# Kernel optimization log

Hardware: AMD Instinct MI355X
Metric: run time of the kernel (lower is better)

The kernel has to match this reference:

```python
import jax, jax.numpy as jnp
import numpy as np

H = 512
V = 8000

def _attn(hidden, enc, W, b, v):
    # hidden: [1,B,H], enc: [T,B,H] -> context [1,B,H]
    encB = jnp.transpose(enc, (1, 0, 2))                      # [B,T,H]
    Hrep = jnp.broadcast_to(jnp.transpose(hidden, (1, 0, 2)), encB.shape)
    energy = jnp.tanh(jnp.concatenate([Hrep, encB], axis=-1) @ W.T + b)  # [B,T,H]
    scores = jnp.einsum('bth,h->bt', energy, v)               # [B,T]
    a = jax.nn.softmax(scores, axis=1)
    ctx = jnp.einsum('bt,bth->bh', a, encB)                   # [B,H]
    return ctx[None]

def _gru_step(x, h, W_ih, W_hh, b_ih, b_hh):
    # x: [B,in], h: [B,H]; PyTorch gate order r,z,n
    gi = x @ W_ih.T + b_ih
    gh = h @ W_hh.T + b_hh
    i_r, i_z, i_n = jnp.split(gi, 3, axis=1)
    h_r, h_z, h_n = jnp.split(gh, 3, axis=1)
    r = jax.nn.sigmoid(i_r + h_r)
    z = jax.nn.sigmoid(i_z + h_z)
    n = jnp.tanh(i_n + r * h_n)
    return (1.0 - z) * n + z * h

def setup_inputs() -> dict:
    key = jax.random.key(0)
    ks = jax.random.split(key, 20)
    B, Tz, Tu, E, D = 128, 64, 128, 512, 5
    gin = E + 2 * H + D  # 1541
    s = 0.02  # small init scale to keep tanh/sigmoid unsaturated
    return {
        'z_enc_out': jax.random.normal(ks[0], (Tz, B, H), jnp.float32),
        'u_enc_out': jax.random.normal(ks[1], (Tu, B, H), jnp.float32),
        'm_t_input': jax.random.randint(ks[2], (1, B), 0, V),
        'degree_input': jax.random.uniform(ks[3], (B, D), jnp.float32),
        'last_hidden': jax.random.normal(ks[4], (1, B, H), jnp.float32),
        'sparse_response': jax.random.uniform(ks[5], (B, Tz, V + Tz), jnp.float32, 1e-3, 1.0),
        'emb_table': jax.random.normal(ks[6], (V, E), jnp.float32) * s,
        'attn_z_W': jax.random.normal(ks[7], (H, 2 * H), jnp.float32) * s,
        'attn_z_b': jnp.zeros((H,), jnp.float32),
        'attn_z_v': jax.random.normal(ks[8], (H,), jnp.float32) * s,
        'attn_u_W': jax.random.normal(ks[9], (H, 2 * H), jnp.float32) * s,
        'attn_u_b': jnp.zeros((H,), jnp.float32),
        'attn_u_v': jax.random.normal(ks[10], (H,), jnp.float32) * s,
        'gru_W_ih': jax.random.normal(ks[11], (3 * H, gin), jnp.float32) * s,
        'gru_W_hh': jax.random.normal(ks[12], (3 * H, H), jnp.float32) * s,
        'gru_b_ih': jnp.zeros((3 * H,), jnp.float32),
        'gru_b_hh': jnp.zeros((3 * H,), jnp.float32),
        'proj_W': jax.random.normal(ks[13], (V, 3 * H), jnp.float32) * s,
        'proj_b': jnp.zeros((V,), jnp.float32),
        'copy2_W': jax.random.normal(ks[14], (H, H), jnp.float32) * s,
        'copy2_b': jnp.zeros((H,), jnp.float32),
    }

def reference(z_enc_out, u_enc_out, m_t_input, degree_input, last_hidden,
              sparse_response, emb_table, attn_z_W, attn_z_b, attn_z_v,
              attn_u_W, attn_u_b, attn_u_v, gru_W_ih, gru_W_hh, gru_b_ih,
              gru_b_hh, proj_W, proj_b, copy2_W, copy2_b):
    m_embed = emb_table[m_t_input]                                 # [1,B,E]
    z_ctx = _attn(last_hidden, z_enc_out, attn_z_W, attn_z_b, attn_z_v)  # [1,B,H]
    u_ctx = _attn(last_hidden, u_enc_out, attn_u_W, attn_u_b, attn_u_v)  # [1,B,H]
    gru_in = jnp.concatenate([m_embed, u_ctx, z_ctx, degree_input[None]], axis=2)
    h_new = _gru_step(gru_in[0], last_hidden[0], gru_W_ih, gru_W_hh, gru_b_ih, gru_b_hh)  # [B,H]
    gru_out = h_new[None]                                          # [1,B,H]
    gen_score = (jnp.concatenate([z_ctx, u_ctx, gru_out], axis=2)[0] @ proj_W.T + proj_b)  # [B,V]
    # copy scores over z encoder positions
    zT = jnp.transpose(z_enc_out, (1, 0, 2))                       # [B,Tz,H]
    cs = jnp.tanh(zT @ copy2_W.T + copy2_b)                        # [B,Tz,H]
    z_score = jnp.einsum('bth,bh->bt', cs, h_new)                  # [B,Tz]
    m = jnp.max(z_score, axis=1, keepdims=True)
    e = jnp.exp(z_score - m)
    z_copy = jnp.log(jnp.einsum('bt,btv->bv', e, sparse_response)) + m  # [B,V+Tz]
    scores = jax.nn.softmax(jnp.concatenate([gen_score, z_copy], axis=1), axis=1)
    gen, cp = scores[:, :V], scores[:, V:]
    proba = jnp.concatenate([gen + cp[:, :V], cp[:, V:]], axis=1)  # [B,V+Tz]
    return proba, gru_out, gru_out
```

## Files before the change

kernel.cpp:

```cpp
#include <hip/hip_runtime.h>
#include <hip/hip_bf16.h>
#include <math.h>

#define B_   128
#define H_   512
#define TZ   64
#define TU   128
#define V_   8000
#define VC   8064
#define GIN  1541
#define GINP 1568
#define G3   1536
#define NB   8

typedef float f32x4 __attribute__((ext_vector_type(4)));
typedef __bf16 bf16x8 __attribute__((ext_vector_type(8)));

__device__ __forceinline__ float sigmoidf_(float x){ return 1.f/(1.f+__expf(-x)); }

__device__ __forceinline__ void cvt8(const float* __restrict__ s, __bf16* __restrict__ d){
  float4 x = *(const float4*)s;
  float4 y = *(const float4*)(s+4);
  bf16x8 r;
  r[0]=(__bf16)x.x; r[1]=(__bf16)x.y; r[2]=(__bf16)x.z; r[3]=(__bf16)x.w;
  r[4]=(__bf16)y.x; r[5]=(__bf16)y.y; r[6]=(__bf16)y.z; r[7]=(__bf16)y.w;
  *(bf16x8*)d = r;
}

#define U_Z   524288u
#define U_U   1048576u
#define U_H   8192u
#define U_ZW  65536u
#define U_UW  65536u
#define U_CW  32768u
#define U_WHH 98304u
#define U_PW  1536000u
#define U_WIH 301056u
#define CVT_UNITS (U_Z+U_U+U_H+U_ZW+U_UW+U_CW+U_WHH+U_PW+U_WIH)

__global__ __launch_bounds__(256) void cvt_all(
    const float* __restrict__ z, const float* __restrict__ u, const float* __restrict__ hid,
    const float* __restrict__ zW, const float* __restrict__ uW, const float* __restrict__ cW,
    const float* __restrict__ whh, const float* __restrict__ pW, const float* __restrict__ wih,
    __bf16* __restrict__ zb, __bf16* __restrict__ ub, __bf16* __restrict__ hb,
    __bf16* __restrict__ zWb, __bf16* __restrict__ uWb, __bf16* __restrict__ cWb,
    __bf16* __restrict__ whhb, __bf16* __restrict__ pWb, __bf16* __restrict__ Wp)
{
  unsigned t = blockIdx.x*256u + threadIdx.x;
  if (t >= CVT_UNITS) return;
  unsigned o = t;
  if (o >= CVT_UNITS - U_WIH) {
    o -= (CVT_UNITS - U_WIH);
    unsigned r = o / (GINP/8), cu = o % (GINP/8);
    int c0 = cu*8;
    const float* src = wih + (size_t)r*GIN;
    bf16x8 v;
#pragma unroll
    for (int e = 0; e < 8; ++e) {
      int c = c0 + e;
      v[e] = (__bf16)((c < GIN) ? src[c] : 0.f);
    }
    *(bf16x8*)(Wp + (size_t)r*GINP + c0) = v;
    return;
  }
  const float* s; __bf16* d;
  if      (o < U_Z)                   { s=z;   d=zb;   }
  else if ((o-=U_Z)   < U_U)          { s=u;   d=ub;   }
  else if ((o-=U_U)   < U_H)          { s=hid; d=hb;   }
  else if ((o-=U_H)   < U_ZW)         { s=zW;  d=zWb;  }
  else if ((o-=U_ZW)  < U_UW)         { s=uW;  d=uWb;  }
  else if ((o-=U_UW)  < U_CW)         { s=cW;  d=cWb;  }
  else if ((o-=U_CW)  < U_WHH)        { s=whh; d=whhb; }
  else     { o-=U_WHH;                  s=pW;  d=pWb;  }
  cvt8(s + (size_t)o*8, d + (size_t)o*8);
}

__global__ __launch_bounds__(256) void hidden3(
    const __bf16* __restrict__ hb,
    const __bf16* __restrict__ zWb, const float* __restrict__ zbias, float* __restrict__ hWz,
    const __bf16* __restrict__ uWb, const float* __restrict__ ubias, float* __restrict__ hWu,
    const __bf16* __restrict__ whhb, const float* __restrict__ hbias, float* __restrict__ gh)
{
  const int wv = threadIdx.x >> 6, lane = threadIdx.x & 63;
  const int tile = blockIdx.x*4 + wv;
  if (tile >= 80) return;
  const __bf16* W; const float* bias; float* C; int ldw, ldc, nbn, lt;
  if (tile < 16)      { W=zWb;  bias=zbias; C=hWz; ldw=2*H_; ldc=H_; nbn=8;  lt=tile; }
  else if (tile < 32) { W=uWb;  bias=ubias; C=hWu; ldw=2*H_; ldc=H_; nbn=8;  lt=tile-16; }
  else                { W=whhb; bias=hbias; C=gh;  ldw=H_;   ldc=G3; nbn=24; lt=tile-32; }
  const int bn = (lt % nbn) * 64, bm = (lt / nbn) * 64;
  const int col = lane & 15, g = lane >> 4;
  f32x4 acc[4][4] = {};
  for (int k0 = 0; k0 < 512; k0 += 32) {
    const int k = k0 + g*8;
    bf16x8 af[4], bw[4];
#pragma unroll
    for (int i = 0; i < 4; ++i) {
      af[i] = *(const bf16x8*)(hb + (size_t)(bm + i*16 + col)*H_ + k);
      bw[i] = *(const bf16x8*)(W  + (size_t)(bn + i*16 + col)*ldw + k);
    }
#pragma unroll
    for (int i = 0; i < 4; ++i)
#pragma unroll
      for (int j = 0; j < 4; ++j)
        acc[i][j] = __builtin_amdgcn_mfma_f32_16x16x32_bf16(af[i], bw[j], acc[i][j], 0, 0, 0);
  }
#pragma unroll
  for (int mi = 0; mi < 4; ++mi)
#pragma unroll
    for (int r = 0; r < 4; ++r) {
      int m = bm + mi*16 + g*4 + r;
#pragma unroll
      for (int ni = 0; ni < 4; ++ni) {
        int n = bn + ni*16 + col;
        C[(size_t)m*ldc + n] = acc[mi][ni][r] + bias[n];
      }
    }
}

__global__ __launch_bounds__(256) void mfma_energy2(
    const __bf16* __restrict__ Az, const __bf16* __restrict__ Wz, int ldwz,
    const float* __restrict__ addz, int asz, const float* __restrict__ mulz, int msz,
    float* __restrict__ outz, int Tz,
    const __bf16* __restrict__ Au, const __bf16* __restrict__ Wu, int ldwu,
    const float* __restrict__ addu, int asu, const float* __restrict__ mulu, int msu,
    float* __restrict__ outu, int Tu,
    int ztiles, int ntiles)
{
  const int wv = threadIdx.x >> 6, lane = threadIdx.x & 63;
  const int tile = blockIdx.x*4 + wv;
  if (tile >= ntiles) return;
  const __bf16 *A, *W; const float *add, *mul; float* outp;
  int ldw, as, ms, T, lt;
  if (tile < ztiles) { A=Az; W=Wz; ldw=ldwz; add=addz; as=asz; mul=mulz; ms=msz; outp=outz; T=Tz; lt=tile; }
  else               { A=Au; W=Wu; ldw=ldwu; add=addu; as=asu; mul=mulu; ms=msu; outp=outu; T=Tu; lt=tile-ztiles; }
  const int nb = lt & 7;
  const int bn = nb * 64, bm = (lt >> 3) * 64;
  const int col = lane & 15, g = lane >> 4;
  f32x4 acc[4][4] = {};
  for (int k0 = 0; k0 < 512; k0 += 32) {
    const int k = k0 + g*8;
    bf16x8 af[4], bw[4];
#pragma unroll
    for (int i = 0; i < 4; ++i) {
      af[i] = *(const bf16x8*)(A + (size_t)(bm + i*16 + col)*512 + k);
      bw[i] = *(const bf16x8*)(W + (size_t)(bn + i*16 + col)*ldw + k);
    }
#pragma unroll
    for (int i = 0; i < 4; ++i)
#pragma unroll
      for (int j = 0; j < 4; ++j)
        acc[i][j] = __builtin_amdgcn_mfma_f32_16x16x32_bf16(af[i], bw[j], acc[i][j], 0, 0, 0);
  }
#pragma unroll
  for (int mi = 0; mi < 4; ++mi)
#pragma unroll
    for (int r = 0; r < 4; ++r) {
      int m = bm + mi*16 + g*4 + r;
      int b = m & (B_-1), t = m >> 7;
      float p = 0.f;
#pragma unroll
      for (int ni = 0; ni < 4; ++ni) {
        int n = bn + ni*16 + col;
        float v = tanhf(acc[mi][ni][r] + add[(size_t)b*as + n]);
        p += v * mul[(size_t)b*ms + n];
      }
      p += __shfl_xor(p, 1); p += __shfl_xor(p, 2);
      p += __shfl_xor(p, 4); p += __shfl_xor(p, 8);
      if (col == 0) outp[(size_t)nb*(B_*T) + b*T + t] = p;
    }
}

__global__ __launch_bounds__(256) void attn_ctx_concat(
    const float* __restrict__ partZ, const float* __restrict__ partU,
    const __bf16* __restrict__ zb, const __bf16* __restrict__ ub,
    const int* __restrict__ m_t, const float* __restrict__ emb,
    const float* __restrict__ degree,
    __bf16* __restrict__ gin, __bf16* __restrict__ cat3b)
{
  const int b = blockIdx.x, tid = threadIdx.x;
  __shared__ float sa[256];
  __shared__ float awz[TZ];
  __shared__ float awu[TU];
  {
    float s = -INFINITY;
    if (tid < TZ) {
      s = 0.f;
#pragma unroll
      for (int nb = 0; nb < NB; ++nb) s += partZ[(size_t)nb*(B_*TZ) + b*TZ + tid];
    }
    sa[tid] = s; __syncthreads();
    for (int o = 128; o > 0; o >>= 1) { if (tid < o) sa[tid] = fmaxf(sa[tid], sa[tid+o]); __syncthreads(); }
    float mx = sa[0]; __syncthreads();
    float e = (tid < TZ) ? __expf(s - mx) : 0.f;
    sa[tid] = e; __syncthreads();
    for (int o = 128; o > 0; o >>= 1) { if (tid < o) sa[tid] += sa[tid+o]; __syncthreads(); }
    float inv = 1.f / sa[0];
    if (tid < TZ) awz[tid] = e * inv;
    __syncthreads();
  }
  {
    float s = -INFINITY;
    if (tid < TU) {
      s = 0.f;
#pragma unroll
      for (int nb = 0; nb < NB; ++nb) s += partU[(size_t)nb*(B_*TU) + b*TU + tid];
    }
    sa[tid] = s; __syncthreads();
    for (int o = 128; o > 0; o >>= 1) { if (tid < o) sa[tid] = fmaxf(sa[tid], sa[tid+o]); __syncthreads(); }
    float mx = sa[0]; __syncthreads();
    float e = (tid < TU) ? __expf(s - mx) : 0.f;
    sa[tid] = e; __syncthreads();
    for (int o = 128; o > 0; o >>= 1) { if (tid < o) sa[tid] += sa[tid+o]; __syncthreads(); }
    float inv = 1.f / sa[0];
    if (tid < TU) awu[tid] = e * inv;
    __syncthreads();
  }
  const float* e = emb + (size_t)m_t[b] * H_;
  for (int h = tid; h < H_; h += 256) {
    float accz = 0.f, accu = 0.f;
    for (int t = 0; t < TZ; ++t) accz += awz[t] * (float)zb[((size_t)t*B_ + b)*H_ + h];
    for (int t = 0; t < TU; ++t) accu += awu[t] * (float)ub[((size_t)t*B_ + b)*H_ + h];
    gin[(size_t)b*GINP + h]          = (__bf16)e[h];
    gin[(size_t)b*GINP + H_ + h]     = (__bf16)accu;
    gin[(size_t)b*GINP + 2*H_ + h]   = (__bf16)accz;
    cat3b[(size_t)b*G3 + h]          = (__bf16)accz;
    cat3b[(size_t)b*G3 + H_ + h]     = (__bf16)accu;
  }
  if (tid < 5) gin[(size_t)b*GINP + 3*H_ + tid] = (__bf16)degree[b*5 + tid];
  if (tid >= 5 && tid < 32) gin[(size_t)b*GINP + GIN + (tid-5)] = (__bf16)0.f;
}

__global__ __launch_bounds__(256) void mfma_gru(
    const __bf16* __restrict__ A, const __bf16* __restrict__ W,
    float* __restrict__ giA, float* __restrict__ giB)
{
  const int wv = threadIdx.x >> 6, lane = threadIdx.x & 63;
  const int tile = blockIdx.x*4 + wv;
  if (tile >= 96) return;
  const int half = tile / 48, lt = tile % 48;
  const int bn = (lt % 24) * 64, bm = (lt / 24) * 64;
  const int col = lane & 15, g = lane >> 4;
  const int kbeg = half ? 800 : 0, kend_ = half ? GINP : 800;
  float* C = half ? giB : giA;
  f32x4 acc[4][4] = {};
  for (int k0 = kbeg; k0 < kend_; k0 += 32) {
    const int k = k0 + g*8;
    bf16x8 af[4], bw[4];
#pragma unroll
    for (int i = 0; i < 4; ++i) {
      af[i] = *(const bf16x8*)(A + (size_t)(bm + i*16 + col)*GINP + k);
      bw[i] = *(const bf16x8*)(W + (size_t)(bn + i*16 + col)*GINP + k);
    }
#pragma unroll
    for (int i = 0; i < 4; ++i)
#pragma unroll
      for (int j = 0; j < 4; ++j)
        acc[i][j] = __builtin_amdgcn_mfma_f32_16x16x32_bf16(af[i], bw[j], acc[i][j], 0, 0, 0);
  }
#pragma unroll
  for (int mi = 0; mi < 4; ++mi)
#pragma unroll
    for (int r = 0; r < 4; ++r) {
      int m = bm + mi*16 + g*4 + r;
#pragma unroll
      for (int ni = 0; ni < 4; ++ni)
        C[(size_t)m*G3 + bn + ni*16 + col] = acc[mi][ni][r];
    }
}

__global__ __launch_bounds__(256) void gru_kernel(
    const float* __restrict__ giA, const float* __restrict__ giB,
    const float* __restrict__ gh, const float* __restrict__ bih,
    const float* __restrict__ hprev,
    float* __restrict__ hnew, __bf16* __restrict__ cat3b,
    float* __restrict__ out1, float* __restrict__ out2)
{
  int idx = blockIdx.x*256 + threadIdx.x;
  int b = idx >> 9, h = idx & (H_-1);
  size_t base = (size_t)b*G3;
  float ir = giA[base + h]        + giB[base + h]        + bih[h]        + gh[base + h];
  float iz = giA[base + H_ + h]   + giB[base + H_ + h]   + bih[H_ + h]   + gh[base + H_ + h];
  float in_= giA[base + 2*H_ + h] + giB[base + 2*H_ + h] + bih[2*H_ + h];
  float hn = gh[base + 2*H_ + h];
  float r = sigmoidf_(ir);
  float z = sigmoidf_(iz);
  float n = tanhf(in_ + r*hn);
  float hv = (1.f - z)*n + z*hprev[idx];
  hnew[idx] = hv;
  cat3b[base + 2*H_ + h] = (__bf16)hv;
  out1[idx] = hv;
  out2[idx] = hv;
}

__global__ __launch_bounds__(256) void proj_copy(
    const __bf16* __restrict__ cat3b, const __bf16* __restrict__ pWb, float* __restrict__ P,
    const __bf16* __restrict__ zb, const __bf16* __restrict__ cWb,
    const float* __restrict__ c2b, const float* __restrict__ hnew,
    float* __restrict__ partC)
{
  const int wv = threadIdx.x >> 6, lane = threadIdx.x & 63;
  const int tile = blockIdx.x*4 + wv;
  const int col = lane & 15, g = lane >> 4;
  if (tile < 750) {
    const int s = tile / 250, t2 = tile % 250;
    const int bn = (t2 % 125) * 64, bm = (t2 / 125) * 64;
    const __bf16* As = cat3b + s*512;
    const __bf16* Ws = pWb + s*512;
    float* C = P + (size_t)s*B_*V_;
    f32x4 acc[4][4] = {};
    for (int k0 = 0; k0 < 512; k0 += 32) {
      const int k = k0 + g*8;
      bf16x8 af[4], bw[4];
#pragma unroll
      for (int i = 0; i < 4; ++i) {
        af[i] = *(const bf16x8*)(As + (size_t)(bm + i*16 + col)*G3 + k);
        bw[i] = *(const bf16x8*)(Ws + (size_t)(bn + i*16 + col)*G3 + k);
      }
#pragma unroll
      for (int i = 0; i < 4; ++i)
#pragma unroll
        for (int j = 0; j < 4; ++j)
          acc[i][j] = __builtin_amdgcn_mfma_f32_16x16x32_bf16(af[i], bw[j], acc[i][j], 0, 0, 0);
    }
#pragma unroll
    for (int mi = 0; mi < 4; ++mi)
#pragma unroll
      for (int r = 0; r < 4; ++r) {
        int m = bm + mi*16 + g*4 + r;
#pragma unroll
        for (int ni = 0; ni < 4; ++ni)
          C[(size_t)m*V_ + bn + ni*16 + col] = acc[mi][ni][r];
      }
  } else if (tile < 750 + 1024) {
    const int lt = tile - 750;
    const int nb = lt & 7;
    const int bn = nb * 64, bm = (lt >> 3) * 64;
    f32x4 acc[4][4] = {};
    for (int k0 = 0; k0 < 512; k0 += 32) {
      const int k = k0 + g*8;
      bf16x8 af[4], bw[4];
#pragma unroll
      for (int i = 0; i < 4; ++i) {
        af[i] = *(const bf16x8*)(zb + (size_t)(bm + i*16 + col)*512 + k);
        bw[i] = *(const bf16x8*)(cWb + (size_t)(bn + i*16 + col)*H_ + k);
      }
#pragma unroll
      for (int i = 0; i < 4; ++i)
#pragma unroll
        for (int j = 0; j < 4; ++j)
          acc[i][j] = __builtin_amdgcn_mfma_f32_16x16x32_bf16(af[i], bw[j], acc[i][j], 0, 0, 0);
    }
#pragma unroll
    for (int mi = 0; mi < 4; ++mi)
#pragma unroll
      for (int r = 0; r < 4; ++r) {
        int m = bm + mi*16 + g*4 + r;
        int b = m & (B_-1), t = m >> 7;
        float p = 0.f;
#pragma unroll
        for (int ni = 0; ni < 4; ++ni) {
          int n = bn + ni*16 + col;
          float v = tanhf(acc[mi][ni][r] + c2b[n]);
          p += v * hnew[(size_t)b*H_ + n];
        }
        p += __shfl_xor(p, 1); p += __shfl_xor(p, 2);
        p += __shfl_xor(p, 4); p += __shfl_xor(p, 8);
        if (col == 0) partC[(size_t)nb*(B_*TZ) + b*TZ + t] = p;
      }
  }
}

__global__ __launch_bounds__(256) void zcopy_kernel(
    const float* __restrict__ partC, const float* __restrict__ sr,
    float* __restrict__ zbuf)
{
  const int b = blockIdx.y, tid = threadIdx.x;
  __shared__ float se[TZ];
  __shared__ float smx;
  if (tid < TZ) {
    float s = 0.f;
#pragma unroll
    for (int nb = 0; nb < NB; ++nb) s += partC[(size_t)nb*(B_*TZ) + b*TZ + tid];
    float mx = s;
    mx = fmaxf(mx, __shfl_xor(mx, 1));  mx = fmaxf(mx, __shfl_xor(mx, 2));
    mx = fmaxf(mx, __shfl_xor(mx, 4));  mx = fmaxf(mx, __shfl_xor(mx, 8));
    mx = fmaxf(mx, __shfl_xor(mx, 16)); mx = fmaxf(mx, __shfl_xor(mx, 32));
    se[tid] = __expf(s - mx);
    if (tid == 0) smx = mx;
  }
  __syncthreads();
  const int v0 = blockIdx.x*1024 + tid*4;
  if (v0 >= VC) return;
  float4 acc = {0.f, 0.f, 0.f, 0.f};
  const float* base = sr + (size_t)b*TZ*VC;
#pragma unroll 4
  for (int t = 0; t < TZ; ++t) {
    float et = se[t];
    float4 x = *(const float4*)(base + (size_t)t*VC + v0);
    acc.x += et*x.x; acc.y += et*x.y; acc.z += et*x.z; acc.w += et*x.w;
  }
  float m = smx;
  float* out = zbuf + (size_t)b*VC + v0;
  out[0] = __logf(acc.x) + m;
  out[1] = __logf(acc.y) + m;
  out[2] = __logf(acc.z) + m;
  out[3] = __logf(acc.w) + m;
}

__global__ __launch_bounds__(256) void final_softmax2(
    const float* __restrict__ p0, const float* __restrict__ p1, const float* __restrict__ p2,
    const float* __restrict__ bias, const float* __restrict__ zbuf, float* __restrict__ out0)
{
  const int b = blockIdx.x, tid = threadIdx.x;
  const float* q0 = p0 + (size_t)b*V_;
  const float* q1 = p1 + (size_t)b*V_;
  const float* q2 = p2 + (size_t)b*V_;
  const float* zr = zbuf + (size_t)b*VC;
  __shared__ float sa[256];
  float mx = -INFINITY;
  for (int i = tid; i < V_; i += 256) mx = fmaxf(mx, q0[i]+q1[i]+q2[i]+bias[i]);
  for (int i = tid; i < VC; i += 256) mx = fmaxf(mx, zr[i]);
  sa[tid] = mx; __syncthreads();
  for (int o = 128; o > 0; o >>= 1) { if (tid < o) sa[tid] = fmaxf(sa[tid], sa[tid+o]); __syncthreads(); }
  mx = sa[0]; __syncthreads();
  float sum = 0.f;
  for (int i = tid; i < V_; i += 256) sum += __expf(q0[i]+q1[i]+q2[i]+bias[i] - mx);
  for (int i = tid; i < VC; i += 256) sum += __expf(zr[i] - mx);
  sa[tid] = sum; __syncthreads();
  for (int o = 128; o > 0; o >>= 1) { if (tid < o) sa[tid] += sa[tid+o]; __syncthreads(); }
  float inv = 1.f / sa[0];
  float* o0 = out0 + (size_t)b*VC;
  for (int j = tid; j < V_; j += 256)
    o0[j] = (__expf(q0[j]+q1[j]+q2[j]+bias[j]-mx) + __expf(zr[j]-mx)) * inv;
  for (int j = tid; j < TZ; j += 256)
    o0[V_ + j] = __expf(zr[V_ + j] - mx) * inv;
}

extern "C" void kernel_launch(void* const* d_in, const int* in_sizes, int n_in,
                              void* d_out, int out_size, void* d_ws, size_t ws_size,
                              hipStream_t stream)
{
  const float* z_enc   = (const float*)d_in[0];
  const float* u_enc   = (const float*)d_in[1];
  const int*   m_t     = (const int*)  d_in[2];
  const float* degree  = (const float*)d_in[3];
  const float* hidden  = (const float*)d_in[4];
  const float* sr      = (const float*)d_in[5];
  const float* emb     = (const float*)d_in[6];
  const float* attn_z_W= (const float*)d_in[7];
  const float* attn_z_b= (const float*)d_in[8];
  const float* attn_z_v= (const float*)d_in[9];
  const float* attn_u_W= (const float*)d_in[10];
  const float* attn_u_b= (const float*)d_in[11];
  const float* attn_u_v= (const float*)d_in[12];
  const float* gru_W_ih= (const float*)d_in[13];
  const float* gru_W_hh= (const float*)d_in[14];
  const float* gru_b_ih= (const float*)d_in[15];
  const float* gru_b_hh= (const float*)d_in[16];
  const float* proj_W  = (const float*)d_in[17];
  const float* proj_b  = (const float*)d_in[18];
  const float* copy2_W = (const float*)d_in[19];
  const float* copy2_b = (const float*)d_in[20];

  float* out0 = (float*)d_out;
  float* out1 = out0 + (size_t)B_*VC;
  float* out2 = out1 + (size_t)B_*H_;

  float* ws    = (float*)d_ws;
  float* hWz   = ws;
  float* hWu   = hWz   + B_*H_;
  float* gh    = hWu   + B_*H_;
  float* partZ = gh    + B_*G3;
  float* partU = partZ + NB*B_*TZ;
  float* partC = partU + NB*B_*TU;
  float* giA   = partC + NB*B_*TZ;
  float* giB   = giA   + B_*G3;
  float* hnew  = giB   + B_*G3;
  float* p0    = hnew  + B_*H_;
  float* p1    = p0    + (size_t)B_*V_;
  float* p2    = p1    + (size_t)B_*V_;
  float* zbuf  = p2    + (size_t)B_*V_;
  __bf16* gin   = (__bf16*)(zbuf + (size_t)B_*VC);
  __bf16* Wp    = gin   + (size_t)B_*GINP;
  __bf16* zb    = Wp    + (size_t)G3*GINP;
  __bf16* ub    = zb    + (size_t)TZ*B_*H_;
  __bf16* hb    = ub    + (size_t)TU*B_*H_;
  __bf16* zWb   = hb    + (size_t)B_*H_;
  __bf16* uWb   = zWb   + (size_t)H_*2*H_;
  __bf16* cWb   = uWb   + (size_t)H_*2*H_;
  __bf16* whhb  = cWb   + (size_t)H_*H_;
  __bf16* pWb   = whhb  + (size_t)G3*H_;
  __bf16* cat3b = pWb   + (size_t)V_*G3;

  cvt_all<<<(CVT_UNITS + 255)/256, 256, 0, stream>>>(
      z_enc, u_enc, hidden, attn_z_W, attn_u_W, copy2_W, gru_W_hh, proj_W, gru_W_ih,
      zb, ub, hb, zWb, uWb, cWb, whhb, pWb, Wp);

  hidden3<<<20, 256, 0, stream>>>(hb, zWb, attn_z_b, hWz, uWb, attn_u_b, hWu, whhb, gru_b_hh, gh);

  mfma_energy2<<<768, 256, 0, stream>>>(
      zb, zWb + H_, 2*H_, hWz, H_, attn_z_v, 0, partZ, TZ,
      ub, uWb + H_, 2*H_, hWu, H_, attn_u_v, 0, partU, TU,
      1024, 3072);

  attn_ctx_concat<<<B_, 256, 0, stream>>>(partZ, partU, zb, ub, m_t, emb, degree, gin, cat3b);

  mfma_gru<<<24, 256, 0, stream>>>(gin, Wp, giA, giB);
  gru_kernel<<<(B_*H_)/256, 256, 0, stream>>>(giA, giB, gh, gru_b_ih, hidden, hnew, cat3b, out1, out2);

  proj_copy<<<444, 256, 0, stream>>>(cat3b, pWb, p0, zb, cWb, copy2_b, hnew, partC);

  zcopy_kernel<<<dim3((VC + 1023)/1024, B_), 256, 0, stream>>>(partC, sr, zbuf);

  final_softmax2<<<B_, 256, 0, stream>>>(p0, p1, p2, proj_b, zbuf, out0);
}
```

Before: 295.2 us.

## Convert projection weights to bf16 inside proj GEMM and cover full batch per tile

Stops pre-converting the large proj_W matrix to bf16 in cvt_all. The projection GEMM now reads fp32 weights directly and converts them in registers. Each wave now covers all 128 batch rows (8x4 MFMA tiles), so every weight tile is loaded once rather than twice. This removes a separate write and re-read of about 24 MB of bf16 weights, at the cost of doubled accumulator registers per wave, fewer tiles and blocks, and fp32 weight loads that are twice as wide.

```diff
diff --git a/kernel.cpp b/kernel.cpp
--- a/kernel.cpp
+++ b/kernel.cpp
@@ -18,13 +18,16 @@
 
 __device__ __forceinline__ float sigmoidf_(float x){ return 1.f/(1.f+__expf(-x)); }
 
-__device__ __forceinline__ void cvt8(const float* __restrict__ s, __bf16* __restrict__ d){
-  float4 x = *(const float4*)s;
-  float4 y = *(const float4*)(s+4);
+__device__ __forceinline__ bf16x8 load8_bf16(const float* __restrict__ p){
+  float4 x = *(const float4*)p;
+  float4 y = *(const float4*)(p+4);
   bf16x8 r;
   r[0]=(__bf16)x.x; r[1]=(__bf16)x.y; r[2]=(__bf16)x.z; r[3]=(__bf16)x.w;
   r[4]=(__bf16)y.x; r[5]=(__bf16)y.y; r[6]=(__bf16)y.z; r[7]=(__bf16)y.w;
-  *(bf16x8*)d = r;
+  return r;
+}
+__device__ __forceinline__ void cvt8(const float* __restrict__ s, __bf16* __restrict__ d){
+  *(bf16x8*)d = load8_bf16(s);
 }
 
 #define U_Z   524288u
@@ -34,17 +37,16 @@
 #define U_UW  65536u
 #define U_CW  32768u
 #define U_WHH 98304u
-#define U_PW  1536000u
 #define U_WIH 301056u
-#define CVT_UNITS (U_Z+U_U+U_H+U_ZW+U_UW+U_CW+U_WHH+U_PW+U_WIH)
+#define CVT_UNITS (U_Z+U_U+U_H+U_ZW+U_UW+U_CW+U_WHH+U_WIH)
 
 __global__ __launch_bounds__(256) void cvt_all(
     const float* __restrict__ z, const float* __restrict__ u, const float* __restrict__ hid,
     const float* __restrict__ zW, const float* __restrict__ uW, const float* __restrict__ cW,
-    const float* __restrict__ whh, const float* __restrict__ pW, const float* __restrict__ wih,
+    const float* __restrict__ whh, const float* __restrict__ wih,
     __bf16* __restrict__ zb, __bf16* __restrict__ ub, __bf16* __restrict__ hb,
     __bf16* __restrict__ zWb, __bf16* __restrict__ uWb, __bf16* __restrict__ cWb,
-    __bf16* __restrict__ whhb, __bf16* __restrict__ pWb, __bf16* __restrict__ Wp)
+    __bf16* __restrict__ whhb, __bf16* __restrict__ Wp)
 {
   unsigned t = blockIdx.x*256u + threadIdx.x;
   if (t >= CVT_UNITS) return;
@@ -70,8 +72,7 @@
   else if ((o-=U_H)   < U_ZW)         { s=zW;  d=zWb;  }
   else if ((o-=U_ZW)  < U_UW)         { s=uW;  d=uWb;  }
   else if ((o-=U_UW)  < U_CW)         { s=cW;  d=cWb;  }
-  else if ((o-=U_CW)  < U_WHH)        { s=whh; d=whhb; }
-  else     { o-=U_WHH;                  s=pW;  d=pWb;  }
+  else     { o-=U_CW;                   s=whh; d=whhb; }
   cvt8(s + (size_t)o*8, d + (size_t)o*8);
 }
 
@@ -294,7 +295,7 @@
 }
 
 __global__ __launch_bounds__(256) void proj_copy(
-    const __bf16* __restrict__ cat3b, const __bf16* __restrict__ pWb, float* __restrict__ P,
+    const __bf16* __restrict__ cat3b, const float* __restrict__ pW, float* __restrict__ P,
     const __bf16* __restrict__ zb, const __bf16* __restrict__ cWb,
     const float* __restrict__ c2b, const float* __restrict__ hnew,
     float* __restrict__ partC)
@@ -302,38 +303,39 @@
   const int wv = threadIdx.x >> 6, lane = threadIdx.x & 63;
   const int tile = blockIdx.x*4 + wv;
   const int col = lane & 15, g = lane >> 4;
-  if (tile < 750) {
-    const int s = tile / 250, t2 = tile % 250;
-    const int bn = (t2 % 125) * 64, bm = (t2 / 125) * 64;
+  if (tile < 375) {
+    const int s = tile / 125;
+    const int bn = (tile % 125) * 64;
     const __bf16* As = cat3b + s*512;
-    const __bf16* Ws = pWb + s*512;
+    const float*  Ws = pW + s*512;
     float* C = P + (size_t)s*B_*V_;
-    f32x4 acc[4][4] = {};
+    f32x4 acc[8][4] = {};
     for (int k0 = 0; k0 < 512; k0 += 32) {
       const int k = k0 + g*8;
-      bf16x8 af[4], bw[4];
-#pragma unroll
-      for (int i = 0; i < 4; ++i) {
-        af[i] = *(const bf16x8*)(As + (size_t)(bm + i*16 + col)*G3 + k);
-        bw[i] = *(const bf16x8*)(Ws + (size_t)(bn + i*16 + col)*G3 + k);
-      }
+      bf16x8 af[8], bw[4];
+#pragma unroll
+      for (int i = 0; i < 8; ++i)
+        af[i] = *(const bf16x8*)(As + (size_t)(i*16 + col)*G3 + k);
 #pragma unroll
       for (int i = 0; i < 4; ++i)
-#pragma unroll
-        for (int j = 0; j < 4; ++j)
-          acc[i][j] = __builtin_amdgcn_mfma_f32_16x16x32_bf16(af[i], bw[j], acc[i][j], 0, 0, 0);
-    }
-#pragma unroll
-    for (int mi = 0; mi < 4; ++mi)
+        bw[i] = load8_bf16(Ws + (size_t)(bn + i*16 + col)*G3 + k);
+#pragma unroll
+      for (int mi = 0; mi < 8; ++mi)
+#pragma unroll
+        for (int ni = 0; ni < 4; ++ni)
+          acc[mi][ni] = __builtin_amdgcn_mfma_f32_16x16x32_bf16(af[mi], bw[ni], acc[mi][ni], 0, 0, 0);
+    }
+#pragma unroll
+    for (int mi = 0; mi < 8; ++mi)
 #pragma unroll
       for (int r = 0; r < 4; ++r) {
-        int m = bm + mi*16 + g*4 + r;
+        int m = mi*16 + g*4 + r;
 #pragma unroll
         for (int ni = 0; ni < 4; ++ni)
           C[(size_t)m*V_ + bn + ni*16 + col] = acc[mi][ni][r];
       }
-  } else if (tile < 750 + 1024) {
-    const int lt = tile - 750;
+  } else if (tile < 375 + 1024) {
+    const int lt = tile - 375;
     const int nb = lt & 7;
     const int bn = nb * 64, bm = (lt >> 3) * 64;
     f32x4 acc[4][4] = {};
@@ -490,12 +492,11 @@
   __bf16* uWb   = zWb   + (size_t)H_*2*H_;
   __bf16* cWb   = uWb   + (size_t)H_*2*H_;
   __bf16* whhb  = cWb   + (size_t)H_*H_;
-  __bf16* pWb   = whhb  + (size_t)G3*H_;
-  __bf16* cat3b = pWb   + (size_t)V_*G3;
+  __bf16* cat3b = whhb  + (size_t)G3*H_;
 
   cvt_all<<<(CVT_UNITS + 255)/256, 256, 0, stream>>>(
-      z_enc, u_enc, hidden, attn_z_W, attn_u_W, copy2_W, gru_W_hh, proj_W, gru_W_ih,
-      zb, ub, hb, zWb, uWb, cWb, whhb, pWb, Wp);
+      z_enc, u_enc, hidden, attn_z_W, attn_u_W, copy2_W, gru_W_hh, gru_W_ih,
+      zb, ub, hb, zWb, uWb, cWb, whhb, Wp);
 
   hidden3<<<20, 256, 0, stream>>>(hb, zWb, attn_z_b, hWz, uWb, attn_u_b, hWu, whhb, gru_b_hh, gh);
 
@@ -509,7 +510,7 @@
   mfma_gru<<<24, 256, 0, stream>>>(gin, Wp, giA, giB);
   gru_kernel<<<(B_*H_)/256, 256, 0, stream>>>(giA, giB, gh, gru_b_ih, hidden, hnew, cat3b, out1, out2);
 
-  proj_copy<<<444, 256, 0, stream>>>(cat3b, pWb, p0, zb, cWb, copy2_b, hnew, partC);
+  proj_copy<<<350, 256, 0, stream>>>(cat3b, proj_W, p0, zb, cWb, copy2_b, hnew, partC);
 
   zcopy_kernel<<<dim3((VC + 1023)/1024, B_), 256, 0, stream>>>(partC, sr, zbuf);
 
```

Measured after the change: 302.1 us. 2.3% more time.

## Fuse hidden-state GEMMs into conversion kernel and vectorize attention context

Applied to the files above, without the earlier changes.

The separate hidden3 GEMM kernel is merged into the conversion kernel. Its blocks read fp32 hidden and weight data directly and convert to bf16 in registers, so the bf16 copies of hidden and W_hh are no longer written or read and one launch goes away. The attention context loop now splits the time dimension across four waves, each lane loading 8 bf16 values at once, and sums the partial results through shared memory. The cost is that the GEMM blocks now re-read fp32 weights, which is twice the bytes per load, and they share a launch with the bandwidth-heavy conversion blocks.

```diff
diff --git a/kernel.cpp b/kernel.cpp
--- a/kernel.cpp
+++ b/kernel.cpp
@@ -18,35 +18,78 @@
 
 __device__ __forceinline__ float sigmoidf_(float x){ return 1.f/(1.f+__expf(-x)); }
 
-__device__ __forceinline__ void cvt8(const float* __restrict__ s, __bf16* __restrict__ d){
-  float4 x = *(const float4*)s;
-  float4 y = *(const float4*)(s+4);
+__device__ __forceinline__ bf16x8 load8_bf16(const float* __restrict__ p){
+  float4 x = *(const float4*)p;
+  float4 y = *(const float4*)(p+4);
   bf16x8 r;
   r[0]=(__bf16)x.x; r[1]=(__bf16)x.y; r[2]=(__bf16)x.z; r[3]=(__bf16)x.w;
   r[4]=(__bf16)y.x; r[5]=(__bf16)y.y; r[6]=(__bf16)y.z; r[7]=(__bf16)y.w;
-  *(bf16x8*)d = r;
+  return r;
+}
+__device__ __forceinline__ void cvt8(const float* __restrict__ s, __bf16* __restrict__ d){
+  *(bf16x8*)d = load8_bf16(s);
 }
 
 #define U_Z   524288u
 #define U_U   1048576u
-#define U_H   8192u
 #define U_ZW  65536u
 #define U_UW  65536u
 #define U_CW  32768u
-#define U_WHH 98304u
 #define U_PW  1536000u
 #define U_WIH 301056u
-#define CVT_UNITS (U_Z+U_U+U_H+U_ZW+U_UW+U_CW+U_WHH+U_PW+U_WIH)
-
-__global__ __launch_bounds__(256) void cvt_all(
+#define CVT_UNITS (U_Z+U_U+U_ZW+U_UW+U_CW+U_PW+U_WIH)
+#define GEMM_BLOCKS 20
+
+__global__ __launch_bounds__(256) void cvt_hidden3(
     const float* __restrict__ z, const float* __restrict__ u, const float* __restrict__ hid,
     const float* __restrict__ zW, const float* __restrict__ uW, const float* __restrict__ cW,
     const float* __restrict__ whh, const float* __restrict__ pW, const float* __restrict__ wih,
-    __bf16* __restrict__ zb, __bf16* __restrict__ ub, __bf16* __restrict__ hb,
+    __bf16* __restrict__ zb, __bf16* __restrict__ ub,
     __bf16* __restrict__ zWb, __bf16* __restrict__ uWb, __bf16* __restrict__ cWb,
-    __bf16* __restrict__ whhb, __bf16* __restrict__ pWb, __bf16* __restrict__ Wp)
-{
-  unsigned t = blockIdx.x*256u + threadIdx.x;
+    __bf16* __restrict__ pWb, __bf16* __restrict__ Wp,
+    const float* __restrict__ zbias, float* __restrict__ hWz,
+    const float* __restrict__ ubias, float* __restrict__ hWu,
+    const float* __restrict__ hbias, float* __restrict__ gh)
+{
+  if (blockIdx.x < GEMM_BLOCKS) {
+    const int wv = threadIdx.x >> 6, lane = threadIdx.x & 63;
+    const int tile = blockIdx.x*4 + wv;
+    if (tile >= 80) return;
+    const float* W; const float* bias; float* C; int ldw, ldc, nbn, lt;
+    if (tile < 16)      { W=zW;  bias=zbias; C=hWz; ldw=2*H_; ldc=H_; nbn=8;  lt=tile; }
+    else if (tile < 32) { W=uW;  bias=ubias; C=hWu; ldw=2*H_; ldc=H_; nbn=8;  lt=tile-16; }
+    else                { W=whh; bias=hbias; C=gh;  ldw=H_;   ldc=G3; nbn=24; lt=tile-32; }
+    const int bn = (lt % nbn) * 64, bm = (lt / nbn) * 64;
+    const int col = lane & 15, g = lane >> 4;
+    f32x4 acc[4][4] = {};
+    for (int k0 = 0; k0 < 512; k0 += 32) {
+      const int k = k0 + g*8;
+      bf16x8 af[4], bw[4];
+#pragma unroll
+      for (int i = 0; i < 4; ++i) {
+        af[i] = load8_bf16(hid + (size_t)(bm + i*16 + col)*H_ + k);
+        bw[i] = load8_bf16(W   + (size_t)(bn + i*16 + col)*ldw + k);
+      }
+#pragma unroll
+      for (int i = 0; i < 4; ++i)
+#pragma unroll
+        for (int j = 0; j < 4; ++j)
+          acc[i][j] = __builtin_amdgcn_mfma_f32_16x16x32_bf16(af[i], bw[j], acc[i][j], 0, 0, 0);
+    }
+#pragma unroll
+    for (int mi = 0; mi < 4; ++mi)
+#pragma unroll
+      for (int r = 0; r < 4; ++r) {
+        int m = bm + mi*16 + g*4 + r;
+#pragma unroll
+        for (int ni = 0; ni < 4; ++ni) {
+          int n = bn + ni*16 + col;
+          C[(size_t)m*ldc + n] = acc[mi][ni][r] + bias[n];
+        }
+      }
+    return;
+  }
+  unsigned t = (blockIdx.x - GEMM_BLOCKS)*256u + threadIdx.x;
   if (t >= CVT_UNITS) return;
   unsigned o = t;
   if (o >= CVT_UNITS - U_WIH) {
@@ -66,56 +109,11 @@
   const float* s; __bf16* d;
   if      (o < U_Z)                   { s=z;   d=zb;   }
   else if ((o-=U_Z)   < U_U)          { s=u;   d=ub;   }
-  else if ((o-=U_U)   < U_H)          { s=hid; d=hb;   }
-  else if ((o-=U_H)   < U_ZW)         { s=zW;  d=zWb;  }
+  else if ((o-=U_U)   < U_ZW)         { s=zW;  d=zWb;  }
   else if ((o-=U_ZW)  < U_UW)         { s=uW;  d=uWb;  }
   else if ((o-=U_UW)  < U_CW)         { s=cW;  d=cWb;  }
-  else if ((o-=U_CW)  < U_WHH)        { s=whh; d=whhb; }
-  else     { o-=U_WHH;                  s=pW;  d=pWb;  }
+  else     { o-=U_CW;                   s=pW;  d=pWb;  }
   cvt8(s + (size_t)o*8, d + (size_t)o*8);
-}
-
-__global__ __launch_bounds__(256) void hidden3(
-    const __bf16* __restrict__ hb,
-    const __bf16* __restrict__ zWb, const float* __restrict__ zbias, float* __restrict__ hWz,
-    const __bf16* __restrict__ uWb, const float* __restrict__ ubias, float* __restrict__ hWu,
-    const __bf16* __restrict__ whhb, const float* __restrict__ hbias, float* __restrict__ gh)
-{
-  const int wv = threadIdx.x >> 6, lane = threadIdx.x & 63;
-  const int tile = blockIdx.x*4 + wv;
-  if (tile >= 80) return;
-  const __bf16* W; const float* bias; float* C; int ldw, ldc, nbn, lt;
-  if (tile < 16)      { W=zWb;  bias=zbias; C=hWz; ldw=2*H_; ldc=H_; nbn=8;  lt=tile; }
-  else if (tile < 32) { W=uWb;  bias=ubias; C=hWu; ldw=2*H_; ldc=H_; nbn=8;  lt=tile-16; }
-  else                { W=whhb; bias=hbias; C=gh;  ldw=H_;   ldc=G3; nbn=24; lt=tile-32; }
-  const int bn = (lt % nbn) * 64, bm = (lt / nbn) * 64;
-  const int col = lane & 15, g = lane >> 4;
-  f32x4 acc[4][4] = {};
-  for (int k0 = 0; k0 < 512; k0 += 32) {
-    const int k = k0 + g*8;
-    bf16x8 af[4], bw[4];
-#pragma unroll
-    for (int i = 0; i < 4; ++i) {
-      af[i] = *(const bf16x8*)(hb + (size_t)(bm + i*16 + col)*H_ + k);
-      bw[i] = *(const bf16x8*)(W  + (size_t)(bn + i*16 + col)*ldw + k);
-    }
-#pragma unroll
-    for (int i = 0; i < 4; ++i)
-#pragma unroll
-      for (int j = 0; j < 4; ++j)
-        acc[i][j] = __builtin_amdgcn_mfma_f32_16x16x32_bf16(af[i], bw[j], acc[i][j], 0, 0, 0);
-  }
-#pragma unroll
-  for (int mi = 0; mi < 4; ++mi)
-#pragma unroll
-    for (int r = 0; r < 4; ++r) {
-      int m = bm + mi*16 + g*4 + r;
-#pragma unroll
-      for (int ni = 0; ni < 4; ++ni) {
-        int n = bn + ni*16 + col;
-        C[(size_t)m*ldc + n] = acc[mi][ni][r] + bias[n];
-      }
-    }
 }
 
 __global__ __launch_bounds__(256) void mfma_energy2(
@@ -182,6 +180,7 @@
   __shared__ float sa[256];
   __shared__ float awz[TZ];
   __shared__ float awu[TU];
+  __shared__ float szcA[H_], szcB[H_], sucA[H_], sucB[H_];
   {
     float s = -INFINITY;
     if (tid < TZ) {
@@ -216,11 +215,29 @@
     if (tid < TU) awu[tid] = e * inv;
     __syncthreads();
   }
+  {
+    const int wvi = tid >> 6, l = tid & 63;
+    const int h0 = l * 8;
+    float a0=0,a1=0,a2=0,a3=0,a4=0,a5=0,a6=0,a7=0;
+    const __bf16* src; const float* aw; int t0, t1; float* dst;
+    if      (wvi == 0) { src=zb; aw=awz; t0=0;  t1=32;  dst=szcA; }
+    else if (wvi == 2) { src=zb; aw=awz; t0=32; t1=64;  dst=szcB; }
+    else if (wvi == 1) { src=ub; aw=awu; t0=0;  t1=64;  dst=sucA; }
+    else               { src=ub; aw=awu; t0=64; t1=128; dst=sucB; }
+    for (int t = t0; t < t1; ++t) {
+      float w = aw[t];
+      bf16x8 v = *(const bf16x8*)(src + ((size_t)t*B_ + b)*H_ + h0);
+      a0 += w*(float)v[0]; a1 += w*(float)v[1]; a2 += w*(float)v[2]; a3 += w*(float)v[3];
+      a4 += w*(float)v[4]; a5 += w*(float)v[5]; a6 += w*(float)v[6]; a7 += w*(float)v[7];
+    }
+    dst[h0+0]=a0; dst[h0+1]=a1; dst[h0+2]=a2; dst[h0+3]=a3;
+    dst[h0+4]=a4; dst[h0+5]=a5; dst[h0+6]=a6; dst[h0+7]=a7;
+  }
+  __syncthreads();
   const float* e = emb + (size_t)m_t[b] * H_;
   for (int h = tid; h < H_; h += 256) {
-    float accz = 0.f, accu = 0.f;
-    for (int t = 0; t < TZ; ++t) accz += awz[t] * (float)zb[((size_t)t*B_ + b)*H_ + h];
-    for (int t = 0; t < TU; ++t) accu += awu[t] * (float)ub[((size_t)t*B_ + b)*H_ + h];
+    float accz = szcA[h] + szcB[h];
+    float accu = sucA[h] + sucB[h];
     gin[(size_t)b*GINP + h]          = (__bf16)e[h];
     gin[(size_t)b*GINP + H_ + h]     = (__bf16)accu;
     gin[(size_t)b*GINP + 2*H_ + h]   = (__bf16)accz;
@@ -485,19 +502,16 @@
   __bf16* Wp    = gin   + (size_t)B_*GINP;
   __bf16* zb    = Wp    + (size_t)G3*GINP;
   __bf16* ub    = zb    + (size_t)TZ*B_*H_;
-  __bf16* hb    = ub    + (size_t)TU*B_*H_;
-  __bf16* zWb   = hb    + (size_t)B_*H_;
+  __bf16* zWb   = ub    + (size_t)TU*B_*H_;
   __bf16* uWb   = zWb   + (size_t)H_*2*H_;
   __bf16* cWb   = uWb   + (size_t)H_*2*H_;
-  __bf16* whhb  = cWb   + (size_t)H_*H_;
-  __bf16* pWb   = whhb  + (size_t)G3*H_;
+  __bf16* pWb   = cWb   + (size_t)H_*H_;
   __bf16* cat3b = pWb   + (size_t)V_*G3;
 
-  cvt_all<<<(CVT_UNITS + 255)/256, 256, 0, stream>>>(
+  cvt_hidden3<<<GEMM_BLOCKS + (CVT_UNITS + 255)/256, 256, 0, stream>>>(
       z_enc, u_enc, hidden, attn_z_W, attn_u_W, copy2_W, gru_W_hh, proj_W, gru_W_ih,
-      zb, ub, hb, zWb, uWb, cWb, whhb, pWb, Wp);
-
-  hidden3<<<20, 256, 0, stream>>>(hb, zWb, attn_z_b, hWz, uWb, attn_u_b, hWu, whhb, gru_b_hh, gh);
+      zb, ub, zWb, uWb, cWb, pWb, Wp,
+      attn_z_b, hWz, attn_u_b, hWu, gru_b_hh, gh);
 
   mfma_energy2<<<768, 256, 0, stream>>>(
       zb, zWb + H_, 2*H_, hWz, H_, attn_z_v, 0, partZ, TZ,
```

Measured after the change: 295.9 us. About the same (+0.2%).
